# Optimization experiments

Hardware: AMD Instinct MI355X
Metric: run time of the kernel (lower is better)

The kernel has to match this reference:

```python
import jax, jax.numpy as jnp
import numpy as np

B, T, H = 32, 512, 1024   # batch, seq, hidden
L = 512                   # max_seq_length (must be <= 512 for rel_pos_bias)
E = 2048                  # hidden * expansion_factor
S = 128                   # shared qk dim
SQRT_S = float(np.sqrt(S))
EPS = 1e-5


def setup_inputs() -> dict:
    key = jax.random.key(0)
    ks = jax.random.split(key, 9)
    return {
        "x": jax.random.normal(ks[0], (B, T, H), jnp.float32),
        "ln_w": jnp.ones((H,), jnp.float32),
        "ln_b": jnp.zeros((H,), jnp.float32),
        "uv_w": jax.random.normal(ks[1], (2 * E + S, H), jnp.float32) * 0.02,  # torch Linear [out,in]
        "uv_b": jnp.zeros((2 * E + S,), jnp.float32),
        "gamma": jax.random.uniform(ks[2], (2, S), jnp.float32),
        "beta": jax.random.uniform(ks[3], (2, S), jnp.float32),
        "w": jax.random.uniform(ks[4], (2 * L - 1,), jnp.float32),  # Toeplitz rel-pos table
        "o_w": jax.random.normal(ks[5], (H, E), jnp.float32) * 0.02,
        "o_b": jnp.zeros((H,), jnp.float32),
    }


def _rope(x):
    # x: [B, T, 2, S]; positions run along the seq dim (dim=1), faithful to GAU.rope
    half = x.shape[-1] // 2
    pos = jnp.arange(x.shape[1], dtype=x.dtype)
    # note: original uses 10000**(+i/half) (increasing freq) — keep it faithful
    inv_freq = 10000.0 ** (jnp.arange(half, dtype=x.dtype) / half)
    sinusoid = pos[:, None] * inv_freq[None, :]          # [T, half]
    sin = jnp.sin(sinusoid)[None, :, None, :]            # [1, T, 1, half]
    cos = jnp.cos(sinusoid)[None, :, None, :]
    x1, x2 = jnp.split(x, 2, axis=-1)
    return jnp.concatenate([x1 * cos - x2 * sin, x2 * cos + x1 * sin], axis=-1)


def reference(x, ln_w, ln_b, uv_w, uv_b, gamma, beta, w, o_w, o_b):
    Tq = x.shape[1]
    shortcut = x  # hidden_size == output_size -> residual
    # LayerNorm
    mu = jnp.mean(x, axis=-1, keepdims=True)
    var = jnp.mean(jnp.square(x - mu), axis=-1, keepdims=True)
    xn = (x - mu) / jnp.sqrt(var + EPS) * ln_w + ln_b
    # fused uv projection + SiLU, then split into gate u, value v, base
    uv = jax.nn.silu(xn @ uv_w.T + uv_b)                  # [B, T, 2E+S]
    u, v, base = uv[..., :E], uv[..., E:2 * E], uv[..., 2 * E:]
    base = base[:, :, None, :] * gamma[None, None] + beta  # [B, T, 2, S]
    base = _rope(base)
    q, k = base[:, :, 0, :], base[:, :, 1, :]             # [B, T, S]
    qk = jnp.einsum('bis,bjs->bij', q, k)                 # [B, T, T]
    # Toeplitz rel-pos bias: bias[i, j] = w[j - i + L - 1]
    rel = jnp.arange(Tq)[None, :] - jnp.arange(Tq)[:, None] + (L - 1)
    bias = w[rel]                                         # [T, T]
    kernel = jnp.square(jax.nn.relu(qk / SQRT_S + bias[None]))  # squared-ReLU attention
    out = u * jnp.einsum('bij,bje->bie', kernel, v)       # gated attention output [B, T, E]
    return out @ o_w.T + o_b + shortcut
```

## Files before the change

### kernel.cpp

```cpp
#include <hip/hip_runtime.h>

typedef unsigned short u16;
typedef __bf16 bf16x8 __attribute__((ext_vector_type(8)));
typedef float f32x4 __attribute__((ext_vector_type(4)));

#define B_ 32
#define T_ 512
#define H_ 1024
#define E_ 2048
#define S_ 128

__device__ inline u16 f2bf(float f) {
  union { float f; unsigned int u; } c; c.f = f;
  unsigned int u = c.u;
  unsigned int r = (u + 0x7FFFu + ((u >> 16) & 1u)) >> 16;
  return (u16)r;
}
__device__ inline float bf2f(u16 h) {
  union { unsigned int u; float f; } c; c.u = ((unsigned int)h) << 16; return c.f;
}
__device__ inline float silu_fast(float v) {
  return v * __builtin_amdgcn_rcpf(1.0f + __expf(-v));
}

__device__ inline void g2lds16(const u16* g, u16* l) {
  __builtin_amdgcn_global_load_lds(
      (const __attribute__((address_space(1))) void*)g,
      (__attribute__((address_space(3))) void*)l, 16, 0, 0);
}

__global__ __launch_bounds__(256) void ln_kernel(const float* __restrict__ x,
                                                 const float* __restrict__ lw,
                                                 const float* __restrict__ lb,
                                                 u16* __restrict__ xn) {
  int row = blockIdx.x;
  int t = threadIdx.x;
  const float4* xr = (const float4*)(x + (size_t)row * H_);
  float4 v = xr[t];
  float s = v.x + v.y + v.z + v.w;
  float ss = v.x * v.x + v.y * v.y + v.z * v.z + v.w * v.w;
  for (int off = 1; off < 64; off <<= 1) {
    s += __shfl_xor(s, off);
    ss += __shfl_xor(ss, off);
  }
  __shared__ float red[8];
  int w = t >> 6, l = t & 63;
  if (l == 0) { red[w] = s; red[4 + w] = ss; }
  __syncthreads();
  s = red[0] + red[1] + red[2] + red[3];
  ss = red[4] + red[5] + red[6] + red[7];
  float mu = s * (1.0f / H_);
  float var = ss * (1.0f / H_) - mu * mu;
  float inv = rsqrtf(var + 1e-5f);
  int i = t * 4;
  ushort4 o;
  o.x = f2bf((v.x - mu) * inv * lw[i] + lb[i]);
  o.y = f2bf((v.y - mu) * inv * lw[i + 1] + lb[i + 1]);
  o.z = f2bf((v.z - mu) * inv * lw[i + 2] + lb[i + 2]);
  o.w = f2bf((v.w - mu) * inv * lw[i + 3] + lb[i + 3]);
  *(ushort4*)(xn + (size_t)row * H_ + i) = o;
}

__global__ void cvt_kernel(const float* __restrict__ in, u16* __restrict__ out, int n4) {
  int i = blockIdx.x * 256 + threadIdx.x;
  if (i < n4) {
    float4 v = ((const float4*)in)[i];
    ushort4 o;
    o.x = f2bf(v.x); o.y = f2bf(v.y); o.z = f2bf(v.z); o.w = f2bf(v.w);
    ((ushort4*)out)[i] = o;
  }
}

__global__ __launch_bounds__(256) void rope_kernel(const float* __restrict__ base,
                                                   const float* __restrict__ gamma,
                                                   const float* __restrict__ beta,
                                                   u16* __restrict__ q,
                                                   u16* __restrict__ k) {
  int row = blockIdx.x * 4 + (threadIdx.x >> 6);
  int s = threadIdx.x & 63;
  int t = row & (T_ - 1);
  const float* bp = base + (size_t)row * S_;
  float b1 = bp[s], b2 = bp[s + 64];
  float q1 = b1 * gamma[s] + beta[s];
  float q2 = b2 * gamma[64 + s] + beta[64 + s];
  float k1 = b1 * gamma[128 + s] + beta[128 + s];
  float k2 = b2 * gamma[192 + s] + beta[192 + s];
  float invf = (float)pow(10000.0, (double)s * (1.0 / 64.0));
  float ph = (float)t * invf;
  float sn, cs;
  sincosf(ph, &sn, &cs);
  size_t o = (size_t)row * S_;
  q[o + s]      = f2bf(q1 * cs - q2 * sn);
  q[o + 64 + s] = f2bf(q2 * cs + q1 * sn);
  k[o + s]      = f2bf(k1 * cs - k2 * sn);
  k[o + 64 + s] = f2bf(k2 * cs + k1 * sn);
}

template <int MODE>
__global__ __launch_bounds__(256)
void gemm_bt(const u16* __restrict__ A, const u16* __restrict__ Bm,
             int K, long long sA, long long sB,
             void* __restrict__ o0, void* __restrict__ o1, void* __restrict__ o2,
             const void* __restrict__ c0, const void* __restrict__ c1, int nb0) {
  __shared__ __attribute__((aligned(16))) u16 lds[32768];
  u16* lsA = lds;
  u16* lsB = lds + 16384;

  const int z = blockIdx.z;
  const u16* Ab = A + (long long)z * sA;
  const u16* Bb = Bm + (long long)z * sB;
  const int m0 = blockIdx.y * 128;
  const int n0 = nb0 + blockIdx.x * 128;
  const int t = threadIdx.x;
  const int w = t >> 6, l = t & 63;
  const int quad = l >> 4, l16 = l & 15;
  const int wm = (w >> 1) * 64, wn = (w & 1) * 64;
  const int srow = t >> 4;
  const int gl = (t & 15) ^ ((t >> 4) & 7);
  const int dst_off = t * 8;
  const int rsw = l16 & 7;

  f32x4 zero = {0.f, 0.f, 0.f, 0.f};
  f32x4 acc[4][4];
  for (int mi = 0; mi < 4; ++mi)
    for (int ni = 0; ni < 4; ++ni) acc[mi][ni] = zero;

  const u16* gA = Ab + ((size_t)(m0 + srow) * K + gl * 8);
  const u16* gB = Bb + ((size_t)(n0 + srow) * K + gl * 8);
  const size_t rK16 = (size_t)16 * K;

  for (int k0 = 0; k0 < K; k0 += 128) {
    __syncthreads();
#pragma unroll
    for (int c = 0; c < 8; ++c)
      g2lds16(gA + k0 + c * rK16, &lsA[c * 2048 + dst_off]);
#pragma unroll
    for (int c = 0; c < 8; ++c)
      g2lds16(gB + k0 + c * rK16, &lsB[c * 2048 + dst_off]);
    __syncthreads();
#pragma unroll
    for (int j = 0; j < 4; ++j) {
      int pg = ((j * 4 + quad) ^ rsw) * 8;
      bf16x8 af[4], bfr[4];
      for (int i = 0; i < 4; ++i) {
        af[i]  = *(const bf16x8*)&lsA[(wm + i * 16 + l16) * 128 + pg];
        bfr[i] = *(const bf16x8*)&lsB[(wn + i * 16 + l16) * 128 + pg];
      }
      for (int mi = 0; mi < 4; ++mi)
        for (int ni = 0; ni < 4; ++ni)
          acc[mi][ni] = __builtin_amdgcn_mfma_f32_16x16x32_bf16(af[mi], bfr[ni], acc[mi][ni], 0, 0, 0);
    }
  }

  for (int mi = 0; mi < 4; ++mi) {
    for (int ni = 0; ni < 4; ++ni) {
      int n = n0 + wn + ni * 16 + l16;
      for (int r = 0; r < 4; ++r) {
        int m = m0 + wm + mi * 16 + quad * 4 + r;
        float a = acc[mi][ni][r];
        if constexpr (MODE == 0) {
          const float* uvb = (const float*)c0;
          ((float*)o2)[(size_t)m * S_ + (n - 2 * E_)] = silu_fast(a + uvb[n]);
        } else if constexpr (MODE == 1) {
          const float* wrel = (const float*)c0;
          float v = a * 0.08838834764831845f + wrel[n - m + 511];
          v = fmaxf(v, 0.0f);
          ((u16*)o0)[(size_t)z * (T_ * T_) + (size_t)m * T_ + n] = f2bf(v * v);
        }
      }
    }
  }
}

#define PH_SYNC()                                        \
  asm volatile("s_waitcnt lgkmcnt(0)" ::: "memory");     \
  __builtin_amdgcn_sched_barrier(0);                     \
  __builtin_amdgcn_s_barrier();                          \
  __builtin_amdgcn_sched_barrier(0);                     \
  __builtin_amdgcn_s_setprio(1);

#define PH_END()                                         \
  __builtin_amdgcn_s_setprio(0);

#define MM2(mA, mB)                                                                                       \
  _Pragma("unroll")                                                                                       \
  for (int ni = 0; ni < 4; ++ni) {                                                                        \
    acc[mA][ni] = __builtin_amdgcn_mfma_f32_16x16x32_bf16(af[mA][0], bfr[ni][0], acc[mA][ni], 0, 0, 0);   \
    acc[mB][ni] = __builtin_amdgcn_mfma_f32_16x16x32_bf16(af[mB][0], bfr[ni][0], acc[mB][ni], 0, 0, 0);   \
  }                                                                                                       \
  _Pragma("unroll")                                                                                       \
  for (int ni = 0; ni < 4; ++ni) {                                                                        \
    acc[mA][ni] = __builtin_amdgcn_mfma_f32_16x16x32_bf16(af[mA][1], bfr[ni][1], acc[mA][ni], 0, 0, 0);   \
    acc[mB][ni] = __builtin_amdgcn_mfma_f32_16x16x32_bf16(af[mB][1], bfr[ni][1], acc[mB][ni], 0, 0, 0);   \
  }

template <int MODE, bool XSWZ>
__global__ __launch_bounds__(512, 2)
void gemm256(const u16* __restrict__ A, const u16* __restrict__ Bm,
             int K, long long sA, long long sB,
             void* __restrict__ o0, void* __restrict__ o1,
             const void* __restrict__ c0, const void* __restrict__ c1) {
  extern __shared__ u16 lds[];

  int bx = blockIdx.x, by = blockIdx.y;
  if constexpr (XSWZ) {
    int gx = gridDim.x;
    int nwg = gx * gridDim.y;
    int hh = by * gx + bx;
    int cpx = nwg >> 3;
    int lid = (hh & 7) * cpx + (hh >> 3);
    bx = lid % gx; by = lid / gx;
  }
  const int z = blockIdx.z;
  const u16* Ab = A + (long long)z * sA;
  const u16* Bb = Bm + (long long)z * sB;
  const int m0 = by * 256;
  const int n0 = bx * 256;
  const int t = threadIdx.x;
  const int w = t >> 6, ln = t & 63;
  const int quad = ln >> 4, l16 = ln & 15;
  const int wm = w >> 2, wn = w & 3;

  const int nkt = K >> 6;

  const int goff = ((t & 7) ^ ((t >> 3) & 7)) * 8;
  const u16* gA = Ab + (size_t)(m0 + (t >> 3)) * K + goff;
  const u16* gB = Bb + (size_t)(n0 + (t >> 3)) * K + goff;
  u16* ldst = lds + t * 8;
  const size_t rK64 = (size_t)64 * K;
  const size_t rK128 = (size_t)128 * K;

  auto SA = [&](int b, int h, int kt) {
    const u16* g = gA + h * rK128 + (size_t)kt * 64;
    u16* d = ldst + b * 16384 + h * 8192;
    g2lds16(g, d);
    g2lds16(g + rK64, d + 4096);
  };
  auto SB = [&](int b, int h, int kt) {
    const u16* g = gB + h * rK128 + (size_t)kt * 64;
    u16* d = ldst + 32768 + b * 16384 + h * 8192;
    g2lds16(g, d);
    g2lds16(g + rK64, d + 4096);
  };

  f32x4 zero = {0.f, 0.f, 0.f, 0.f};
  f32x4 acc[8][4];
#pragma unroll
  for (int mi = 0; mi < 8; ++mi)
#pragma unroll
    for (int ni = 0; ni < 4; ++ni) acc[mi][ni] = zero;

  SA(0, 0, 0); SA(0, 1, 0); SB(0, 0, 0); SB(0, 1, 0);
  if (nkt > 1) {
    SB(1, 0, 1); SB(1, 1, 1); SA(1, 0, 1);
    asm volatile("s_waitcnt vmcnt(6)" ::: "memory");
  } else {
    asm volatile("s_waitcnt vmcnt(0)" ::: "memory");
  }
  __builtin_amdgcn_s_barrier();

  const u16* lA0 = lds + wm * 8192 + l16 * 64;
  const u16* lB0 = lds + 32768 + (wn >> 1) * 8192 + ((wn & 1) * 64 + l16) * 64;
  const int pg0 = (quad ^ (l16 & 7)) * 8;
  const int pg1 = ((4 + quad) ^ (l16 & 7)) * 8;

  bf16x8 bfr[4][2];
  bf16x8 af[8][2];

  for (int kt = 0; kt < nkt; ++kt) {
    const int b = kt & 1;
    const u16* lA = lA0 + b * 16384;
    const u16* lB = lB0 + b * 16384;
    const bool s2 = (kt + 2 < nkt);

#pragma unroll
    for (int ni = 0; ni < 4; ++ni) {
      bfr[ni][0] = *(const bf16x8*)&lB[ni * 1024 + pg0];
      bfr[ni][1] = *(const bf16x8*)&lB[ni * 1024 + pg1];
    }
#pragma unroll
    for (int mi = 0; mi < 2; ++mi) {
      af[mi][0] = *(const bf16x8*)&lA[mi * 1024 + pg0];
      af[mi][1] = *(const bf16x8*)&lA[mi * 1024 + pg1];
    }
    if (kt + 1 < nkt) SA(b ^ 1, 1, kt + 1);
    PH_SYNC();
    MM2(0, 1);
    PH_END();

#pragma unroll
    for (int mi = 2; mi < 6; ++mi) {
      af[mi][0] = *(const bf16x8*)&lA[mi * 1024 + pg0];
      af[mi][1] = *(const bf16x8*)&lA[mi * 1024 + pg1];
    }
    if (s2) SB(b, 0, kt + 2);
    PH_SYNC();
    MM2(2, 3);
    PH_END();

#pragma unroll
    for (int mi = 6; mi < 8; ++mi) {
      af[mi][0] = *(const bf16x8*)&lA[mi * 1024 + pg0];
      af[mi][1] = *(const bf16x8*)&lA[mi * 1024 + pg1];
    }
    if (s2) SB(b, 1, kt + 2);
    PH_SYNC();
    MM2(4, 5);
    PH_END();

    if (s2) {
      SA(b, 0, kt + 2);
      asm volatile("s_waitcnt vmcnt(6)" ::: "memory");
    } else {
      asm volatile("s_waitcnt vmcnt(0)" ::: "memory");
    }
    __builtin_amdgcn_sched_barrier(0);
    __builtin_amdgcn_s_barrier();
    __builtin_amdgcn_sched_barrier(0);
    __builtin_amdgcn_s_setprio(1);
    MM2(6, 7);
    PH_END();
  }

  if constexpr (MODE == 0) {
    const float* uvb = (const float*)c0;
    if (n0 < E_) {
#pragma unroll
      for (int ni = 0; ni < 4; ++ni) {
        int nl = wn * 64 + ni * 16 + l16;
        float bias = uvb[n0 + nl];
        int g = nl >> 3, o = nl & 7;
#pragma unroll
        for (int mi = 0; mi < 8; ++mi)
#pragma unroll
          for (int r = 0; r < 4; ++r) {
            int ml = wm * 128 + mi * 16 + quad * 4 + r;
            lds[ml * 256 + ((g ^ (ml & 7)) << 3) + o] =
                f2bf(silu_fast(acc[mi][ni][r] + bias));
          }
      }
      __syncthreads();
      u16* o0p = (u16*)o0;
#pragma unroll
      for (int cc = 0; cc < 16; ++cc) {
        int gidx = cc * 512 + t;
        int row = gidx >> 5, gc = gidx & 31;
        uint4 val = *(const uint4*)&lds[row * 256 + ((gc ^ (row & 7)) << 3)];
        *(uint4*)&o0p[(size_t)(m0 + row) * E_ + n0 + gc * 8] = val;
      }
    } else {
      const int bb = m0 >> 9;
      const int tt0 = m0 & (T_ - 1);
      const int nv0 = n0 - E_;
#pragma unroll
      for (int ni = 0; ni < 4; ++ni) {
        int nl = wn * 64 + ni * 16 + l16;
        float bias = uvb[n0 + nl];
#pragma unroll
        for (int mi = 0; mi < 8; ++mi)
#pragma unroll
          for (int r = 0; r < 4; ++r) {
            int ml = wm * 128 + mi * 16 + quad * 4 + r;
            u16 sv = f2bf(silu_fast(acc[mi][ni][r] + bias));
            int g = ml >> 3, o = ml & 7;
            lds[nl * 256 + ((g ^ (nl & 7)) << 3) + o] = sv;
          }
      }
      __syncthreads();
      int row = t >> 1;
      u16* o1p = (u16*)o1;
      size_t gbase = ((size_t)bb * E_ + nv0 + row) * T_ + tt0;
#pragma unroll
      for (int cc = 0; cc < 16; ++cc) {
        int c = (t & 1) * 16 + cc;
        int gs = c ^ (row & 7);
        uint4 val = *(const uint4*)&lds[row * 256 + gs * 8];
        *(uint4*)&o1p[gbase + c * 8] = val;
      }
    }
  } else if constexpr (MODE == 2) {
#pragma unroll
    for (int ni = 0; ni < 4; ++ni) {
      int nl = wn * 64 + ni * 16 + l16;
      int g = nl >> 3, o = nl & 7;
#pragma unroll
      for (int mi = 0; mi < 8; ++mi)
#pragma unroll
        for (int r = 0; r < 4; ++r) {
          int ml = wm * 128 + mi * 16 + quad * 4 + r;
          lds[ml * 256 + ((g ^ (ml & 7)) << 3) + o] = f2bf(acc[mi][ni][r]);
        }
    }
    __syncthreads();
    const u16* uu = (const u16*)c0;
    u16* o0p = (u16*)o0;
#pragma unroll
    for (int cc = 0; cc < 16; ++cc) {
      int gidx = cc * 512 + t;
      int row = gidx >> 5, gc = gidx & 31;
      union { uint4 v; u16 h[8]; } av, uv_, rv;
      av.v = *(const uint4*)&lds[row * 256 + ((gc ^ (row & 7)) << 3)];
      size_t gi = ((size_t)z * T_ + m0 + row) * E_ + n0 + gc * 8;
      uv_.v = *(const uint4*)&uu[gi];
#pragma unroll
      for (int k = 0; k < 8; ++k)
        rv.h[k] = f2bf(bf2f(av.h[k]) * bf2f(uv_.h[k]));
      *(uint4*)&o0p[gi] = rv.v;
    }
  } else {
    const float* ob = (const float*)c0;
    const float* xs = (const float*)c1;
#pragma unroll
    for (int ni = 0; ni < 4; ++ni) {
      int n = n0 + wn * 64 + ni * 16 + l16;
      float bias = ob[n];
#pragma unroll
      for (int mi = 0; mi < 8; ++mi)
#pragma unroll
        for (int r = 0; r < 4; ++r) {
          int m = m0 + wm * 128 + mi * 16 + quad * 4 + r;
          size_t gi = (size_t)m * H_ + n;
          ((float*)o0)[gi] = acc[mi][ni][r] + bias + xs[gi];
        }
    }
  }
}

extern "C" void kernel_launch(void* const* d_in, const int* in_sizes, int n_in,
                              void* d_out, int out_size, void* d_ws, size_t ws_size,
                              hipStream_t stream) {
  const float* x     = (const float*)d_in[0];
  const float* ln_w  = (const float*)d_in[1];
  const float* ln_b  = (const float*)d_in[2];
  const float* uv_w  = (const float*)d_in[3];
  const float* uv_b  = (const float*)d_in[4];
  const float* gamma = (const float*)d_in[5];
  const float* beta  = (const float*)d_in[6];
  const float* wrel  = (const float*)d_in[7];
  const float* o_w   = (const float*)d_in[8];
  const float* o_b   = (const float*)d_in[9];

  char* ws = (char*)d_ws;
  u16*   xn   = (u16*)(ws);
  u16*   qb   = (u16*)(ws);
  u16*   kb   = (u16*)(ws + 4194304);
  u16*   km   = (u16*)(ws + 8388608);
  u16*   uvwb = (u16*)(ws + 33554432);
  u16*   owb  = (u16*)(ws + 42205184);
  u16*   u    = (u16*)(ws + 46399488);
  u16*   vt   = (u16*)(ws + 113508352);
  float* base = (float*)(ws + 180617216);
  u16*   attn = u;

  static int ldsset = -1;
  if (ldsset < 0) {
    auto* k0 = gemm256<0, true>;
    auto* k2 = gemm256<2, false>;
    auto* k3 = gemm256<3, true>;
    hipFuncSetAttribute((const void*)k0, hipFuncAttributeMaxDynamicSharedMemorySize, 131072);
    hipFuncSetAttribute((const void*)k2, hipFuncAttributeMaxDynamicSharedMemorySize, 131072);
    hipFuncSetAttribute((const void*)k3, hipFuncAttributeMaxDynamicSharedMemorySize, 131072);
    ldsset = 1;
  }

  ln_kernel<<<16384, 256, 0, stream>>>(x, ln_w, ln_b, xn);
  cvt_kernel<<<4224, 256, 0, stream>>>(uv_w, uvwb, 4224 * 1024 / 4);
  cvt_kernel<<<2048, 256, 0, stream>>>(o_w, owb, 1024 * 2048 / 4);

  gemm256<0, true><<<dim3(16, 64, 1), 512, 131072, stream>>>(
      xn, uvwb, 1024, 0, 0, u, vt, uv_b, nullptr);
  gemm_bt<0><<<dim3(1, 128, 1), 256, 0, stream>>>(
      xn, uvwb, 1024, 0, 0, nullptr, nullptr, base, uv_b, nullptr, 4096);
  rope_kernel<<<4096, 256, 0, stream>>>(base, gamma, beta, qb, kb);
  gemm_bt<1><<<dim3(4, 4, 32), 256, 0, stream>>>(
      qb, kb, 128, 65536, 65536, km, nullptr, nullptr, wrel, nullptr, 0);
  gemm256<2, false><<<dim3(8, 2, 32), 512, 131072, stream>>>(
      km, vt, 512, 262144, 1048576, attn, nullptr, u, nullptr);
  gemm256<3, true><<<dim3(4, 64, 1), 512, 131072, stream>>>(
      attn, owb, 2048, 0, 0, d_out, nullptr, o_b, x);
}
```

Measured before the change: 519.7 us.

## Restructure GEMM main loop into two-half K pipeline with single barrier

The 256-tile GEMM main loop drops the four-phase schedule, which had 2-stage-ahead prefetch and a barrier per phase. It now uses a simpler double-buffer scheme: prefetch the whole next K tile, and overlap the second K-half MFMAs of the previous iteration with LDS fragment loads of the current one. This removes three workgroup barriers per iteration and interleaves LDS reads with MFMA work. The cost is shallower global prefetch, since it now waits for vmcnt(0) every iteration, which may expose memory latency.

```diff
diff --git a/kernel.cpp b/kernel.cpp
--- a/kernel.cpp
+++ b/kernel.cpp
@@ -172,27 +172,14 @@
   }
 }
 
-#define PH_SYNC()                                        \
-  asm volatile("s_waitcnt lgkmcnt(0)" ::: "memory");     \
-  __builtin_amdgcn_sched_barrier(0);                     \
-  __builtin_amdgcn_s_barrier();                          \
-  __builtin_amdgcn_sched_barrier(0);                     \
-  __builtin_amdgcn_s_setprio(1);
-
-#define PH_END()                                         \
+#define MMH(h)                                                                                            \
+  __builtin_amdgcn_s_setprio(1);                                                                          \
+  _Pragma("unroll")                                                                                       \
+  for (int ni = 0; ni < 4; ++ni)                                                                          \
+    _Pragma("unroll")                                                                                     \
+    for (int mi = 0; mi < 8; ++mi)                                                                        \
+      acc[mi][ni] = __builtin_amdgcn_mfma_f32_16x16x32_bf16(af[mi][h], bfr[ni][h], acc[mi][ni], 0, 0, 0); \
   __builtin_amdgcn_s_setprio(0);
-
-#define MM2(mA, mB)                                                                                       \
-  _Pragma("unroll")                                                                                       \
-  for (int ni = 0; ni < 4; ++ni) {                                                                        \
-    acc[mA][ni] = __builtin_amdgcn_mfma_f32_16x16x32_bf16(af[mA][0], bfr[ni][0], acc[mA][ni], 0, 0, 0);   \
-    acc[mB][ni] = __builtin_amdgcn_mfma_f32_16x16x32_bf16(af[mB][0], bfr[ni][0], acc[mB][ni], 0, 0, 0);   \
-  }                                                                                                       \
-  _Pragma("unroll")                                                                                       \
-  for (int ni = 0; ni < 4; ++ni) {                                                                        \
-    acc[mA][ni] = __builtin_amdgcn_mfma_f32_16x16x32_bf16(af[mA][1], bfr[ni][1], acc[mA][ni], 0, 0, 0);   \
-    acc[mB][ni] = __builtin_amdgcn_mfma_f32_16x16x32_bf16(af[mB][1], bfr[ni][1], acc[mB][ni], 0, 0, 0);   \
-  }
 
 template <int MODE, bool XSWZ>
 __global__ __launch_bounds__(512, 2)
@@ -251,12 +238,7 @@
     for (int ni = 0; ni < 4; ++ni) acc[mi][ni] = zero;
 
   SA(0, 0, 0); SA(0, 1, 0); SB(0, 0, 0); SB(0, 1, 0);
-  if (nkt > 1) {
-    SB(1, 0, 1); SB(1, 1, 1); SA(1, 0, 1);
-    asm volatile("s_waitcnt vmcnt(6)" ::: "memory");
-  } else {
-    asm volatile("s_waitcnt vmcnt(0)" ::: "memory");
-  }
+  asm volatile("s_waitcnt vmcnt(0)" ::: "memory");
   __builtin_amdgcn_s_barrier();
 
   const u16* lA0 = lds + wm * 8192 + l16 * 64;
@@ -271,56 +253,35 @@
     const int b = kt & 1;
     const u16* lA = lA0 + b * 16384;
     const u16* lB = lB0 + b * 16384;
-    const bool s2 = (kt + 2 < nkt);
-
-#pragma unroll
-    for (int ni = 0; ni < 4; ++ni) {
+
+#pragma unroll
+    for (int ni = 0; ni < 4; ++ni)
       bfr[ni][0] = *(const bf16x8*)&lB[ni * 1024 + pg0];
+#pragma unroll
+    for (int mi = 0; mi < 8; ++mi)
+      af[mi][0] = *(const bf16x8*)&lA[mi * 1024 + pg0];
+    if (kt + 1 < nkt) {
+      SA(b ^ 1, 0, kt + 1); SA(b ^ 1, 1, kt + 1);
+      SB(b ^ 1, 0, kt + 1); SB(b ^ 1, 1, kt + 1);
+    }
+    if (kt > 0) { MMH(1); }
+    asm volatile("s_waitcnt lgkmcnt(0)" ::: "memory");
+    __builtin_amdgcn_sched_barrier(0);
+
+#pragma unroll
+    for (int ni = 0; ni < 4; ++ni)
       bfr[ni][1] = *(const bf16x8*)&lB[ni * 1024 + pg1];
-    }
-#pragma unroll
-    for (int mi = 0; mi < 2; ++mi) {
-      af[mi][0] = *(const bf16x8*)&lA[mi * 1024 + pg0];
+#pragma unroll
+    for (int mi = 0; mi < 8; ++mi)
       af[mi][1] = *(const bf16x8*)&lA[mi * 1024 + pg1];
-    }
-    if (kt + 1 < nkt) SA(b ^ 1, 1, kt + 1);
-    PH_SYNC();
-    MM2(0, 1);
-    PH_END();
-
-#pragma unroll
-    for (int mi = 2; mi < 6; ++mi) {
-      af[mi][0] = *(const bf16x8*)&lA[mi * 1024 + pg0];
-      af[mi][1] = *(const bf16x8*)&lA[mi * 1024 + pg1];
-    }
-    if (s2) SB(b, 0, kt + 2);
-    PH_SYNC();
-    MM2(2, 3);
-    PH_END();
-
-#pragma unroll
-    for (int mi = 6; mi < 8; ++mi) {
-      af[mi][0] = *(const bf16x8*)&lA[mi * 1024 + pg0];
-      af[mi][1] = *(const bf16x8*)&lA[mi * 1024 + pg1];
-    }
-    if (s2) SB(b, 1, kt + 2);
-    PH_SYNC();
-    MM2(4, 5);
-    PH_END();
-
-    if (s2) {
-      SA(b, 0, kt + 2);
-      asm volatile("s_waitcnt vmcnt(6)" ::: "memory");
-    } else {
-      asm volatile("s_waitcnt vmcnt(0)" ::: "memory");
-    }
+    MMH(0);
+    asm volatile("s_waitcnt lgkmcnt(0)" ::: "memory");
+    asm volatile("s_waitcnt vmcnt(0)" ::: "memory");
     __builtin_amdgcn_sched_barrier(0);
     __builtin_amdgcn_s_barrier();
     __builtin_amdgcn_sched_barrier(0);
-    __builtin_amdgcn_s_setprio(1);
-    MM2(6, 7);
-    PH_END();
-  }
+  }
+  MMH(1);
 
   if constexpr (MODE == 0) {
     const float* uvb = (const float*)c0;
```

New measurement: 475.5 us. 1.09x faster.
